# Optimization experiments

Hardware: AMD Instinct MI355X
Metric: run time of the kernel (lower is better)

The kernel has to match this reference:

```python
import jax, jax.numpy as jnp
import numpy as np

B = 1024          # number of graphs (subjects)
N1_PER = 116      # nodes per graph, branch 1 (AAL atlas)
N2_PER = 200      # nodes per graph, branch 2 (CC200 atlas)
DEG = 16          # sparsified adjacency degree
H = 32            # hidden_dim
NUM_CLASSES = 2


def _make_graph(key, b, n, deg):
    """Block-diagonal sparse adjacency in COO form, deg edges per node within its block."""
    N = b * n
    E = N * deg
    rows = jnp.repeat(jnp.arange(N, dtype=jnp.int32), deg)
    offs = jax.random.randint(jax.random.fold_in(key, 0), (E,), 0, n, dtype=jnp.int32)
    cols = (rows // n) * n + offs
    vals = jax.random.uniform(jax.random.fold_in(key, 1), (E,), dtype=jnp.float32)
    return rows, cols, vals


def setup_inputs() -> dict:
    key = jax.random.key(0)
    ks = jax.random.split(key, 20)
    rows1, cols1, vals1 = _make_graph(ks[0], B, N1_PER, DEG)
    rows2, cols2, vals2 = _make_graph(ks[1], B, N2_PER, DEG)
    x1 = jax.random.normal(ks[2], (B * N1_PER, N1_PER), dtype=jnp.float32)
    x2 = jax.random.normal(ks[3], (B * N2_PER, N2_PER), dtype=jnp.float32)
    s = 0.1
    inp = {
        "rows1": rows1, "cols1": cols1, "vals1": vals1, "x1": x1,
        "rows2": rows2, "cols2": cols2, "vals2": vals2, "x2": x2,
        # GCN branch 116
        "W1a": jax.random.normal(ks[4], (N1_PER, H), dtype=jnp.float32) * s,
        "b1a": jnp.zeros((H,), jnp.float32),
        "W1b": jax.random.normal(ks[5], (H, H), dtype=jnp.float32) * s,
        "b1b": jnp.zeros((H,), jnp.float32),
        # GCN branch 200
        "W2a": jax.random.normal(ks[6], (N2_PER, H), dtype=jnp.float32) * s,
        "b2a": jnp.zeros((H,), jnp.float32),
        "W2b": jax.random.normal(ks[7], (H, H), dtype=jnp.float32) * s,
        "b2b": jnp.zeros((H,), jnp.float32),
        # MLP head (stored as (in, out))
        "fc1_W": jax.random.normal(ks[8], (4 * H, H), dtype=jnp.float32) * s,
        "fc1_b": jnp.zeros((H,), jnp.float32),
        "fc2_W": jax.random.normal(ks[9], (H, H // 2), dtype=jnp.float32) * s,
        "fc2_b": jnp.zeros((H // 2,), jnp.float32),
        "fc3_W": jax.random.normal(ks[10], (H // 2, NUM_CLASSES), dtype=jnp.float32) * s,
        "fc3_b": jnp.zeros((NUM_CLASSES,), jnp.float32),
    }
    return inp


def _gcn(rows, cols, vals, x, W, b):
    # support = X @ W  (dense GEMM), then sparse aggregation A @ support, then bias
    support = x @ W                              # [N, H]
    msg = vals[:, None] * support[cols]          # gather + scale, [E, H]
    agg = jax.ops.segment_sum(msg, rows, num_segments=x.shape[0])  # scatter-add
    return agg + b


def _branch(rows, cols, vals, x, Wa, ba, Wb, bb, n_per):
    h = jax.nn.relu(_gcn(rows, cols, vals, x, Wa, ba))
    h = jax.nn.relu(_gcn(rows, cols, vals, h, Wb, bb))
    h = h.reshape(-1, n_per, h.shape[-1])        # [B, n, H]
    return jnp.concatenate([h.mean(axis=1), h.max(axis=1)], axis=1)  # [B, 2H]


def reference(rows1, cols1, vals1, x1, rows2, cols2, vals2, x2,
              W1a, b1a, W1b, b1b, W2a, b2a, W2b, b2b,
              fc1_W, fc1_b, fc2_W, fc2_b, fc3_W, fc3_b):
    f116 = _branch(rows1, cols1, vals1, x1, W1a, b1a, W1b, b1b, N1_PER)
    f200 = _branch(rows2, cols2, vals2, x2, W2a, b2a, W2b, b2b, N2_PER)
    x = jnp.concatenate([f116, f200], axis=1)    # [B, 4H]
    h = jax.nn.relu(x @ fc1_W + fc1_b)           # dropout is identity at inference
    h = jax.nn.relu(h @ fc2_W + fc2_b)
    logits = h @ fc3_W + fc3_b                   # [B, 2]
    return logits
```

## Files before the change

### kernel.cpp

```cpp
#include <hip/hip_runtime.h>

#define NB 1024
#define N1P 116
#define N2P 200
#define HD 32
#define T1 464
#define T2 800


template <int ST>
__device__ __forceinline__ void agg_phase(int base, int NPv,
                                          const int* __restrict__ cols,
                                          const float* __restrict__ vals,
                                          const float* __restrict__ sup,
                                          float bias, float* __restrict__ outh,
                                          int tid) {
    const int h = tid & 31;
    for (int n = tid >> 5; n < NPv; n += 8) {
        const int4* c4 = (const int4*)(cols + ((size_t)base + n) * 16);
        const float4* v4 = (const float4*)(vals + ((size_t)base + n) * 16);
        float a = bias;
#pragma unroll
        for (int q = 0; q < 4; ++q) {
            const int4 c = c4[q];
            const float4 v = v4[q];
            a += v.x * sup[(c.x - base) * ST + h];
            a += v.y * sup[(c.y - base) * ST + h];
            a += v.z * sup[(c.z - base) * ST + h];
            a += v.w * sup[(c.w - base) * ST + h];
        }
        outh[n * ST + h] = fmaxf(a, 0.f);
    }
}

template <int K>
__device__ void gemm1_tile(const float* __restrict__ xg,
                           const float* __restrict__ W,
                           float* __restrict__ Sout, float* sX) {
    constexpr int KC = 16;
    constexpr int SXS = 20;
    constexpr int NC = (K + KC - 1) / KC;
    const int tid = threadIdx.x;

    float acc[32];
#pragma unroll
    for (int c = 0; c < 32; ++c) acc[c] = 0.f;

    float4 cur[4];
    auto load_chunk = [&](int kc) {
        const int k0 = kc * KC;
        const int kw = (K - k0) < KC ? (K - k0) : KC;
        const int pieces = kw >> 2;
#pragma unroll
        for (int q = 0; q < 4; ++q) {
            const int i = tid + q * 256;
            const int row = i >> 2, p = i & 3;
            float4 v = make_float4(0.f, 0.f, 0.f, 0.f);
            if (p < pieces)
                v = *(const float4*)(xg + (size_t)row * K + k0 + p * 4);
            cur[q] = v;
        }
    };

    load_chunk(0);
#pragma unroll 1
    for (int kc = 0; kc < NC; ++kc) {
        float* sb = sX + (kc & 1) * (256 * SXS);
#pragma unroll
        for (int q = 0; q < 4; ++q) {
            const int i = tid + q * 256;
            *(float4*)&sb[(i >> 2) * SXS + (i & 3) * 4] = cur[q];
        }
        __syncthreads();
        if (kc + 1 < NC) load_chunk(kc + 1);
        const int k0 = kc * KC;
        const int kw = (K - k0) < KC ? (K - k0) : KC;
        const float* xrow = &sb[tid * SXS];
        const float* wb0 = W + (size_t)k0 * 32;
#pragma unroll 1
        for (int k4 = 0; k4 < kw; k4 += 4) {
            const float4 x4 = *(const float4*)&xrow[k4];
#pragma unroll
            for (int kk = 0; kk < 4; ++kk) {
                const float xs = (&x4.x)[kk];
                const float* w = wb0 + (k4 + kk) * 32;
#pragma unroll
                for (int c4 = 0; c4 < 8; ++c4) {
                    const float4 wv = *(const float4*)&w[c4 * 4];
                    acc[c4 * 4 + 0] += xs * wv.x;
                    acc[c4 * 4 + 1] += xs * wv.y;
                    acc[c4 * 4 + 2] += xs * wv.z;
                    acc[c4 * 4 + 3] += xs * wv.w;
                }
            }
        }
    }

    float* srow = Sout + (size_t)tid * 32;
#pragma unroll
    for (int c4 = 0; c4 < 8; ++c4) {
        float4 o;
        o.x = acc[c4 * 4 + 0]; o.y = acc[c4 * 4 + 1];
        o.z = acc[c4 * 4 + 2]; o.w = acc[c4 * 4 + 3];
        *(float4*)&srow[c4 * 4] = o;
    }
}

__global__ __launch_bounds__(256, 4) void gemm1_kernel(
        const float* __restrict__ x1, const float* __restrict__ W1a,
        float* __restrict__ S1,
        const float* __restrict__ x2, const float* __restrict__ W2a,
        float* __restrict__ S2) {
    __shared__ float sX[2 * 256 * 20];
    const int bid = blockIdx.x;
    if (bid < T1) {
        gemm1_tile<N1P>(x1 + (size_t)bid * 256 * N1P, W1a,
                        S1 + (size_t)bid * 256 * 32, sX);
    } else {
        const int t = bid - T1;
        gemm1_tile<N2P>(x2 + (size_t)t * 256 * N2P, W2a,
                        S2 + (size_t)t * 256 * 32, sX);
    }
}

template <int NP>
__device__ void graph_phase(int g, const float* __restrict__ S,
                            const int* __restrict__ cols,
                            const float* __restrict__ vals,
                            const float* __restrict__ ba,
                            const float* __restrict__ Wb,
                            const float* __restrict__ bb,
                            float* __restrict__ feats, int foff,
                            float* sSup, float* sH) {
    constexpr int ST = 33;
    const int tid = threadIdx.x;
    const int base = g * NP;
    const float bA = ba[tid & 31];
    const float bB = bb[tid & 31];

    const float* Sg = S + (size_t)base * 32;
    constexpr int PIECES = NP * 8;
    constexpr int PSL = (PIECES + 255) / 256;
#pragma unroll
    for (int q = 0; q < PSL; ++q) {
        const int i = tid + q * 256;
        if (i < PIECES) {
            const float4 v = *(const float4*)(Sg + (size_t)i * 4);
            *(float4*)&sSup[(i >> 3) * ST + (i & 7) * 4] = v;
        }
    }
    __syncthreads();

    agg_phase<ST>(base, NP, cols, vals, sSup, bA, sH, tid);
    __syncthreads();

    if (tid < NP) {
        float acc2[32];
#pragma unroll
        for (int c = 0; c < 32; ++c) acc2[c] = 0.f;
        const float* xrow = &sH[tid * ST];
#pragma unroll 1
        for (int k4 = 0; k4 < 32; k4 += 4) {
            const float4 x4 = *(const float4*)&xrow[k4];
#pragma unroll
            for (int kk = 0; kk < 4; ++kk) {
                const float xs = (&x4.x)[kk];
                const float* w = Wb + (k4 + kk) * 32;
#pragma unroll
                for (int c4 = 0; c4 < 8; ++c4) {
                    const float4 wv = *(const float4*)&w[c4 * 4];
                    acc2[c4 * 4 + 0] += xs * wv.x;
                    acc2[c4 * 4 + 1] += xs * wv.y;
                    acc2[c4 * 4 + 2] += xs * wv.z;
                    acc2[c4 * 4 + 3] += xs * wv.w;
                }
            }
        }
#pragma unroll
        for (int c4 = 0; c4 < 8; ++c4) {
            float4 o;
            o.x = acc2[c4 * 4 + 0]; o.y = acc2[c4 * 4 + 1];
            o.z = acc2[c4 * 4 + 2]; o.w = acc2[c4 * 4 + 3];
            *(float4*)&sSup[tid * ST + c4 * 4] = o;
        }
    }
    __syncthreads();

    agg_phase<ST>(base, NP, cols, vals, sSup, bB, sH, tid);
    __syncthreads();

    const int h = tid & 31, sl = tid >> 5;
    float sum = 0.f, mx = -1e30f;
    for (int n = sl; n < NP; n += 8) {
        const float v = sH[n * ST + h];
        sum += v;
        mx = fmaxf(mx, v);
    }
    float* sS = sSup;
    float* sM = sSup + 256;
    sS[tid] = sum;
    sM[tid] = mx;
    __syncthreads();
    if (tid < 32) {
#pragma unroll
        for (int q = 1; q < 8; ++q) {
            sum += sS[tid + 32 * q];
            mx = fmaxf(mx, sM[tid + 32 * q]);
        }
        feats[(size_t)g * 128 + foff + tid] = sum * (1.0f / NP);
        feats[(size_t)g * 128 + foff + 32 + tid] = mx;
    }
}

__global__ __launch_bounds__(256, 3) void graph_fused(
        const float* __restrict__ S1, const int* __restrict__ cols1,
        const float* __restrict__ vals1, const float* __restrict__ b1a,
        const float* __restrict__ W1b, const float* __restrict__ b1b,
        const float* __restrict__ S2, const int* __restrict__ cols2,
        const float* __restrict__ vals2, const float* __restrict__ b2a,
        const float* __restrict__ W2b, const float* __restrict__ b2b,
        float* __restrict__ feats) {
    __shared__ float sSup[N2P * 33];
    __shared__ float sH[N2P * 33];
    const int bid = blockIdx.x;
    const int g = bid >> 1;
    if ((bid & 1) == 0)
        graph_phase<N1P>(g, S1, cols1, vals1, b1a, W1b, b1b, feats, 0, sSup, sH);
    else
        graph_phase<N2P>(g, S2, cols2, vals2, b2a, W2b, b2b, feats, 64, sSup, sH);
}

template <int NP>
__device__ void branch_graph(int g,
                             const float* __restrict__ X,
                             const int* __restrict__ cols,
                             const float* __restrict__ vals,
                             const float* __restrict__ Wa,
                             const float* __restrict__ ba,
                             const float* __restrict__ Wb,
                             const float* __restrict__ bb,
                             float* __restrict__ feats, int foff,
                             float* sSup, float* sH) {
    constexpr int ST = 33;
    constexpr int KC = 16;
    constexpr int SXS = 20;
    constexpr int NSLOT = NP * 4;
    constexpr int PSL = (NSLOT + 255) / 256;

    const int tid = threadIdx.x;
    const int base = g * NP;
    const float* xg = X + (size_t)base * NP;
    const float bA = ba[tid & 31];
    const float bB = bb[tid & 31];

    float* sX = sSup;

    float acc[32];
#pragma unroll
    for (int c = 0; c < 32; ++c) acc[c] = 0.f;

    const int NC = (NP + KC - 1) / KC;

    float4 cur[PSL], nxt[PSL];

    auto load_chunk = [&](int kc, float4* buf) {
        const int k0 = kc * KC;
        const int kw = (NP - k0) < KC ? (NP - k0) : KC;
        const int pieces = kw >> 2;
#pragma unroll
        for (int q = 0; q < PSL; ++q) {
            const int i = tid + q * 256;
            float4 v = make_float4(0.f, 0.f, 0.f, 0.f);
            if (i < NSLOT) {
                const int row = i >> 2, p = i & 3;
                if (p < pieces)
                    v = *(const float4*)(xg + (size_t)row * NP + k0 + p * 4);
            }
            buf[q] = v;
        }
    };
    auto store_chunk = [&](const float4* buf) {
#pragma unroll
        for (int q = 0; q < PSL; ++q) {
            const int i = tid + q * 256;
            if (i < NSLOT) {
                const int row = i >> 2, p = i & 3;
                *(float4*)&sX[row * SXS + p * 4] = buf[q];
            }
        }
    };

    load_chunk(0, cur);
#pragma unroll 1
    for (int kc = 0; kc < NC; ++kc) {
        __syncthreads();
        store_chunk(cur);
        __syncthreads();
        if (kc + 1 < NC) load_chunk(kc + 1, nxt);
        const int k0 = kc * KC;
        const int kw = (NP - k0) < KC ? (NP - k0) : KC;
        if (tid < NP) {
            const float* xrow = &sX[tid * SXS];
            const float* wb0 = Wa + (size_t)k0 * 32;
#pragma unroll 1
            for (int k4 = 0; k4 < kw; k4 += 4) {
                const float4 x4 = *(const float4*)&xrow[k4];
#pragma unroll
                for (int kk = 0; kk < 4; ++kk) {
                    const float xs = (&x4.x)[kk];
                    const float* w = wb0 + (k4 + kk) * 32;
#pragma unroll
                    for (int c4 = 0; c4 < 8; ++c4) {
                        const float4 wv = *(const float4*)&w[c4 * 4];
                        acc[c4 * 4 + 0] += xs * wv.x;
                        acc[c4 * 4 + 1] += xs * wv.y;
                        acc[c4 * 4 + 2] += xs * wv.z;
                        acc[c4 * 4 + 3] += xs * wv.w;
                    }
                }
            }
        }
#pragma unroll
        for (int q = 0; q < PSL; ++q) cur[q] = nxt[q];
    }
    __syncthreads();

    if (tid < NP) {
#pragma unroll
        for (int c4 = 0; c4 < 8; ++c4) {
            float4 o;
            o.x = acc[c4 * 4 + 0]; o.y = acc[c4 * 4 + 1];
            o.z = acc[c4 * 4 + 2]; o.w = acc[c4 * 4 + 3];
            *(float4*)&sSup[tid * ST + c4 * 4] = o;
        }
    }
    __syncthreads();

    agg_phase<ST>(base, NP, cols, vals, sSup, bA, sH, tid);
    __syncthreads();

    if (tid < NP) {
        float acc2[32];
#pragma unroll
        for (int c = 0; c < 32; ++c) acc2[c] = 0.f;
        const float* xrow = &sH[tid * ST];
#pragma unroll 1
        for (int k4 = 0; k4 < 32; k4 += 4) {
            const float4 x4 = *(const float4*)&xrow[k4];
#pragma unroll
            for (int kk = 0; kk < 4; ++kk) {
                const float xs = (&x4.x)[kk];
                const float* w = Wb + (k4 + kk) * 32;
#pragma unroll
                for (int c4 = 0; c4 < 8; ++c4) {
                    const float4 wv = *(const float4*)&w[c4 * 4];
                    acc2[c4 * 4 + 0] += xs * wv.x;
                    acc2[c4 * 4 + 1] += xs * wv.y;
                    acc2[c4 * 4 + 2] += xs * wv.z;
                    acc2[c4 * 4 + 3] += xs * wv.w;
                }
            }
        }
#pragma unroll
        for (int c4 = 0; c4 < 8; ++c4) {
            float4 o;
            o.x = acc2[c4 * 4 + 0]; o.y = acc2[c4 * 4 + 1];
            o.z = acc2[c4 * 4 + 2]; o.w = acc2[c4 * 4 + 3];
            *(float4*)&sSup[tid * ST + c4 * 4] = o;
        }
    }
    __syncthreads();

    agg_phase<ST>(base, NP, cols, vals, sSup, bB, sH, tid);
    __syncthreads();

    const int h = tid & 31, sl = tid >> 5;
    float sum = 0.f, mx = -1e30f;
    for (int n = sl; n < NP; n += 8) {
        const float v = sH[n * ST + h];
        sum += v;
        mx = fmaxf(mx, v);
    }
    float* sS = sSup;
    float* sM = sSup + 256;
    sS[tid] = sum;
    sM[tid] = mx;
    __syncthreads();
    if (tid < 32) {
#pragma unroll
        for (int q = 1; q < 8; ++q) {
            sum += sS[tid + 32 * q];
            mx = fmaxf(mx, sM[tid + 32 * q]);
        }
        feats[(size_t)g * 128 + foff + tid] = sum * (1.0f / NP);
        feats[(size_t)g * 128 + foff + 32 + tid] = mx;
    }
}

__global__ __launch_bounds__(256, 3) void fused_branches(
        const float* __restrict__ x1, const int* __restrict__ cols1,
        const float* __restrict__ vals1,
        const float* __restrict__ W1a, const float* __restrict__ b1a,
        const float* __restrict__ W1b, const float* __restrict__ b1b,
        const float* __restrict__ x2, const int* __restrict__ cols2,
        const float* __restrict__ vals2,
        const float* __restrict__ W2a, const float* __restrict__ b2a,
        const float* __restrict__ W2b, const float* __restrict__ b2b,
        float* __restrict__ feats) {
    __shared__ float sSup[N2P * 33];
    __shared__ float sH[N2P * 33];
    const int bid = blockIdx.x;
    if (bid < NB) {
        branch_graph<N1P>(bid, x1, cols1, vals1, W1a, b1a, W1b, b1b, feats, 0,
                          sSup, sH);
    } else {
        branch_graph<N2P>(bid - NB, x2, cols2, vals2, W2a, b2a, W2b, b2b, feats,
                          64, sSup, sH);
    }
}

__global__ __launch_bounds__(256) void mlp_head(const float* __restrict__ feats,
                                                const float* __restrict__ W1,
                                                const float* __restrict__ b1,
                                                const float* __restrict__ W2,
                                                const float* __restrict__ b2,
                                                const float* __restrict__ W3,
                                                const float* __restrict__ b3,
                                                float* __restrict__ out) {
    __shared__ float sW1[128 * 32];
    __shared__ float sW2[32 * 16];
    __shared__ float sW3[16 * 2];
    __shared__ float sB1[32], sB2[16], sB3[2];
    __shared__ float sF[8 * 128];
    __shared__ float sH1[8 * 32];
    __shared__ float sH2[8 * 16];

    const int tid = threadIdx.x;
    for (int idx = tid; idx < 128 * 32; idx += 256) sW1[idx] = W1[idx];
    for (int idx = tid; idx < 32 * 16; idx += 256) sW2[idx] = W2[idx];
    if (tid < 32) { sW3[tid] = W3[tid]; sB1[tid] = b1[tid]; }
    if (tid < 16) sB2[tid] = b2[tid];
    if (tid < 2) sB3[tid] = b3[tid];
    const long g0 = (long)blockIdx.x * 8;
    for (int idx = tid; idx < 1024; idx += 256) sF[idx] = feats[g0 * 128 + idx];
    __syncthreads();

    const int g = tid >> 5, h = tid & 31;
    float a1 = sB1[h];
#pragma unroll 4
    for (int k = 0; k < 128; ++k) a1 += sF[g * 128 + k] * sW1[k * 32 + h];
    sH1[g * 32 + h] = fmaxf(a1, 0.f);
    __syncthreads();

    if (h < 16) {
        float a2 = sB2[h];
#pragma unroll
        for (int k = 0; k < 32; ++k) a2 += sH1[g * 32 + k] * sW2[k * 16 + h];
        sH2[g * 16 + h] = fmaxf(a2, 0.f);
    }
    __syncthreads();

    if (h < 2) {
        float a3 = sB3[h];
#pragma unroll
        for (int k = 0; k < 16; ++k) a3 += sH2[g * 16 + k] * sW3[k * 2 + h];
        out[(g0 + g) * 2 + h] = a3;
    }
}

extern "C" void kernel_launch(void* const* d_in, const int* in_sizes, int n_in,
                              void* d_out, int out_size, void* d_ws, size_t ws_size,
                              hipStream_t stream) {
    const int*   cols1 = (const int*)d_in[1];
    const float* vals1 = (const float*)d_in[2];
    const float* x1    = (const float*)d_in[3];
    const int*   cols2 = (const int*)d_in[5];
    const float* vals2 = (const float*)d_in[6];
    const float* x2    = (const float*)d_in[7];
    const float* W1a = (const float*)d_in[8];
    const float* b1a = (const float*)d_in[9];
    const float* W1b = (const float*)d_in[10];
    const float* b1b = (const float*)d_in[11];
    const float* W2a = (const float*)d_in[12];
    const float* b2a = (const float*)d_in[13];
    const float* W2b = (const float*)d_in[14];
    const float* b2b = (const float*)d_in[15];
    const float* fc1_W = (const float*)d_in[16];
    const float* fc1_b = (const float*)d_in[17];
    const float* fc2_W = (const float*)d_in[18];
    const float* fc2_b = (const float*)d_in[19];
    const float* fc3_W = (const float*)d_in[20];
    const float* fc3_b = (const float*)d_in[21];
    float* out = (float*)d_out;

    float* feats = (float*)d_ws;
    const size_t FEATS_N = (size_t)NB * 128;
    const size_t S1_N = (size_t)NB * N1P * 32;
    const size_t S2_N = (size_t)NB * N2P * 32;
    const size_t need = (FEATS_N + S1_N + S2_N) * sizeof(float);

    if (ws_size >= need) {
        float* S1 = feats + FEATS_N;
        float* S2 = S1 + S1_N;
        gemm1_kernel<<<T1 + T2, 256, 0, stream>>>(x1, W1a, S1, x2, W2a, S2);
        graph_fused<<<2 * NB, 256, 0, stream>>>(
            S1, cols1, vals1, b1a, W1b, b1b,
            S2, cols2, vals2, b2a, W2b, b2b, feats);
    } else {
        fused_branches<<<2 * NB, 256, 0, stream>>>(
            x1, cols1, vals1, W1a, b1a, W1b, b1b,
            x2, cols2, vals2, W2a, b2a, W2b, b2b, feats);
    }

    mlp_head<<<NB / 8, 256, 0, stream>>>(feats, fc1_W, fc1_b, fc2_W, fc2_b,
                                         fc3_W, fc3_b, out);
}
```

Before: 495.3 us.

## Use direct global-to-LDS loads in gemm1 and drop second LDS buffer in graph kernel

The first-layer GEMM now stages X tiles with global_load_lds (direct global-to-LDS DMA), using an XOR swizzle instead of padded rows and a register round-trip, and raises the occupancy hint. The graph kernel keeps first-layer aggregation results in registers, reuses one shared buffer instead of two, and fuses the second aggregation with the mean/max pooling. It also splits the sums into four independent accumulators. Halving shared memory lets more blocks fit per CU, at the cost of extra barriers and more register pressure.

Result: slower. 860.0 us (+73.6%).

```diff
diff --git a/kernel.cpp b/kernel.cpp
--- a/kernel.cpp
+++ b/kernel.cpp
@@ -1,4 +1,5 @@
 #include <hip/hip_runtime.h>
+#include <stdint.h>
 
 #define NB 1024
 #define N1P 116
@@ -8,29 +9,10 @@
 #define T2 800
 
 
-template <int ST>
-__device__ __forceinline__ void agg_phase(int base, int NPv,
-                                          const int* __restrict__ cols,
-                                          const float* __restrict__ vals,
-                                          const float* __restrict__ sup,
-                                          float bias, float* __restrict__ outh,
-                                          int tid) {
-    const int h = tid & 31;
-    for (int n = tid >> 5; n < NPv; n += 8) {
-        const int4* c4 = (const int4*)(cols + ((size_t)base + n) * 16);
-        const float4* v4 = (const float4*)(vals + ((size_t)base + n) * 16);
-        float a = bias;
-#pragma unroll
-        for (int q = 0; q < 4; ++q) {
-            const int4 c = c4[q];
-            const float4 v = v4[q];
-            a += v.x * sup[(c.x - base) * ST + h];
-            a += v.y * sup[(c.y - base) * ST + h];
-            a += v.z * sup[(c.z - base) * ST + h];
-            a += v.w * sup[(c.w - base) * ST + h];
-        }
-        outh[n * ST + h] = fmaxf(a, 0.f);
-    }
+__device__ __forceinline__ void gll16(const void* g, void* l) {
+    __builtin_amdgcn_global_load_lds(
+        (const __attribute__((address_space(1))) void*)g,
+        (__attribute__((address_space(3))) void*)l, 16, 0, 0);
 }
 
 template <int K>
@@ -38,62 +20,64 @@
                            const float* __restrict__ W,
                            float* __restrict__ Sout, float* sX) {
     constexpr int KC = 16;
-    constexpr int SXS = 20;
     constexpr int NC = (K + KC - 1) / KC;
     const int tid = threadIdx.x;
+    const int lane = tid & 63;
+    const int wave = tid >> 6;
+    const int ris = lane >> 2;
+    const int pq = lane & 3;
 
     float acc[32];
 #pragma unroll
     for (int c = 0; c < 32; ++c) acc[c] = 0.f;
 
-    float4 cur[4];
-    auto load_chunk = [&](int kc) {
+    auto issue = [&](int kc, int buf) {
+        const int k0 = kc * KC;
+        const int pieces = ((K - k0) < KC ? (K - k0) : KC) >> 2;
+#pragma unroll
+        for (int i = 0; i < 4; ++i) {
+            const int s = wave * 4 + i;
+            const int row = s * 16 + ris;
+            const int g = pq ^ ((row >> 1) & 3);
+            if (g < pieces)
+                gll16(xg + (size_t)row * K + k0 + g * 4,
+                      sX + buf * 4096 + s * 256);
+        }
+    };
+
+    issue(0, 0);
+    __syncthreads();
+
+    const int sw = (tid >> 1) & 3;
+    int buf = 0;
+#pragma unroll 1
+    for (int kc = 0; kc < NC; ++kc) {
+        if (kc + 1 < NC) issue(kc + 1, buf ^ 1);
         const int k0 = kc * KC;
         const int kw = (K - k0) < KC ? (K - k0) : KC;
-        const int pieces = kw >> 2;
-#pragma unroll
-        for (int q = 0; q < 4; ++q) {
-            const int i = tid + q * 256;
-            const int row = i >> 2, p = i & 3;
-            float4 v = make_float4(0.f, 0.f, 0.f, 0.f);
-            if (p < pieces)
-                v = *(const float4*)(xg + (size_t)row * K + k0 + p * 4);
-            cur[q] = v;
-        }
-    };
-
-    load_chunk(0);
-#pragma unroll 1
-    for (int kc = 0; kc < NC; ++kc) {
-        float* sb = sX + (kc & 1) * (256 * SXS);
-#pragma unroll
-        for (int q = 0; q < 4; ++q) {
-            const int i = tid + q * 256;
-            *(float4*)&sb[(i >> 2) * SXS + (i & 3) * 4] = cur[q];
+        const float* xrow = sX + buf * 4096 + tid * 16;
+#pragma unroll
+        for (int G = 0; G < 4; ++G) {
+            if (G * 4 < kw) {
+                const float4 x4 = *(const float4*)&xrow[(G ^ sw) * 4];
+                const float* wb = W + (size_t)(k0 + G * 4) * 32;
+#pragma unroll
+                for (int kk = 0; kk < 4; ++kk) {
+                    const float xs = (&x4.x)[kk];
+                    const float* w = wb + kk * 32;
+#pragma unroll
+                    for (int c4 = 0; c4 < 8; ++c4) {
+                        const float4 wv = *(const float4*)&w[c4 * 4];
+                        acc[c4 * 4 + 0] += xs * wv.x;
+                        acc[c4 * 4 + 1] += xs * wv.y;
+                        acc[c4 * 4 + 2] += xs * wv.z;
+                        acc[c4 * 4 + 3] += xs * wv.w;
+                    }
+                }
+            }
         }
         __syncthreads();
-        if (kc + 1 < NC) load_chunk(kc + 1);
-        const int k0 = kc * KC;
-        const int kw = (K - k0) < KC ? (K - k0) : KC;
-        const float* xrow = &sb[tid * SXS];
-        const float* wb0 = W + (size_t)k0 * 32;
-#pragma unroll 1
-        for (int k4 = 0; k4 < kw; k4 += 4) {
-            const float4 x4 = *(const float4*)&xrow[k4];
-#pragma unroll
-            for (int kk = 0; kk < 4; ++kk) {
-                const float xs = (&x4.x)[kk];
-                const float* w = wb0 + (k4 + kk) * 32;
-#pragma unroll
-                for (int c4 = 0; c4 < 8; ++c4) {
-                    const float4 wv = *(const float4*)&w[c4 * 4];
-                    acc[c4 * 4 + 0] += xs * wv.x;
-                    acc[c4 * 4 + 1] += xs * wv.y;
-                    acc[c4 * 4 + 2] += xs * wv.z;
-                    acc[c4 * 4 + 3] += xs * wv.w;
-                }
-            }
-        }
+        buf ^= 1;
     }
 
     float* srow = Sout + (size_t)tid * 32;
@@ -106,12 +90,12 @@
     }
 }
 
-__global__ __launch_bounds__(256, 4) void gemm1_kernel(
+__global__ __launch_bounds__(256, 5) void gemm1_kernel(
         const float* __restrict__ x1, const float* __restrict__ W1a,
         float* __restrict__ S1,
         const float* __restrict__ x2, const float* __restrict__ W2a,
         float* __restrict__ S2) {
-    __shared__ float sX[2 * 256 * 20];
+    __shared__ float sX[2 * 4096];
     const int bid = blockIdx.x;
     if (bid < T1) {
         gemm1_tile<N1P>(x1 + (size_t)bid * 256 * N1P, W1a,
@@ -131,12 +115,14 @@
                             const float* __restrict__ Wb,
                             const float* __restrict__ bb,
                             float* __restrict__ feats, int foff,
-                            float* sSup, float* sH) {
+                            float* sSup) {
     constexpr int ST = 33;
+    constexpr int NI = (NP + 7) / 8;
     const int tid = threadIdx.x;
+    const int h = tid & 31, sl = tid >> 5;
     const int base = g * NP;
-    const float bA = ba[tid & 31];
-    const float bB = bb[tid & 31];
+    const float bA = ba[h];
+    const float bB = bb[h];
 
     const float* Sg = S + (size_t)base * 32;
     constexpr int PIECES = NP * 8;
@@ -151,15 +137,41 @@
     }
     __syncthreads();
 
-    agg_phase<ST>(base, NP, cols, vals, sSup, bA, sH, tid);
-    __syncthreads();
-
+    float hr[NI];
+#pragma unroll
+    for (int i = 0; i < NI; ++i) {
+        const int n = sl + i * 8;
+        if (NP % 8 == 0 || n < NP) {
+            const int4* c4 = (const int4*)(cols + ((size_t)(base + n)) * 16);
+            const float4* v4 = (const float4*)(vals + ((size_t)(base + n)) * 16);
+            float a0 = 0.f, a1 = 0.f, a2 = 0.f, a3 = 0.f;
+#pragma unroll
+            for (int q = 0; q < 4; ++q) {
+                const int4 c = c4[q];
+                const float4 v = v4[q];
+                a0 += v.x * sSup[(c.x - base) * ST + h];
+                a1 += v.y * sSup[(c.y - base) * ST + h];
+                a2 += v.z * sSup[(c.z - base) * ST + h];
+                a3 += v.w * sSup[(c.w - base) * ST + h];
+            }
+            hr[i] = fmaxf(bA + ((a0 + a1) + (a2 + a3)), 0.f);
+        }
+    }
+    __syncthreads();
+
+#pragma unroll
+    for (int i = 0; i < NI; ++i) {
+        const int n = sl + i * 8;
+        if (NP % 8 == 0 || n < NP) sSup[n * ST + h] = hr[i];
+    }
+    __syncthreads();
+
+    float acc2[32];
     if (tid < NP) {
-        float acc2[32];
 #pragma unroll
         for (int c = 0; c < 32; ++c) acc2[c] = 0.f;
-        const float* xrow = &sH[tid * ST];
-#pragma unroll 1
+        const float* xrow = &sSup[tid * ST];
+#pragma unroll
         for (int k4 = 0; k4 < 32; k4 += 4) {
             const float4 x4 = *(const float4*)&xrow[k4];
 #pragma unroll
@@ -176,6 +188,10 @@
                 }
             }
         }
+    }
+    __syncthreads();
+
+    if (tid < NP) {
 #pragma unroll
         for (int c4 = 0; c4 < 8; ++c4) {
             float4 o;
@@ -186,33 +202,45 @@
     }
     __syncthreads();
 
-    agg_phase<ST>(base, NP, cols, vals, sSup, bB, sH, tid);
-    __syncthreads();
-
-    const int h = tid & 31, sl = tid >> 5;
     float sum = 0.f, mx = -1e30f;
-    for (int n = sl; n < NP; n += 8) {
-        const float v = sH[n * ST + h];
-        sum += v;
-        mx = fmaxf(mx, v);
-    }
-    float* sS = sSup;
-    float* sM = sSup + 256;
-    sS[tid] = sum;
-    sM[tid] = mx;
+#pragma unroll
+    for (int i = 0; i < NI; ++i) {
+        const int n = sl + i * 8;
+        if (NP % 8 == 0 || n < NP) {
+            const int4* c4 = (const int4*)(cols + ((size_t)(base + n)) * 16);
+            const float4* v4 = (const float4*)(vals + ((size_t)(base + n)) * 16);
+            float a0 = 0.f, a1 = 0.f, a2 = 0.f, a3 = 0.f;
+#pragma unroll
+            for (int q = 0; q < 4; ++q) {
+                const int4 c = c4[q];
+                const float4 v = v4[q];
+                a0 += v.x * sSup[(c.x - base) * ST + h];
+                a1 += v.y * sSup[(c.y - base) * ST + h];
+                a2 += v.z * sSup[(c.z - base) * ST + h];
+                a3 += v.w * sSup[(c.w - base) * ST + h];
+            }
+            const float v2 = fmaxf(bB + ((a0 + a1) + (a2 + a3)), 0.f);
+            sum += v2;
+            mx = fmaxf(mx, v2);
+        }
+    }
+    __syncthreads();
+
+    sSup[tid] = sum;
+    sSup[256 + tid] = mx;
     __syncthreads();
     if (tid < 32) {
 #pragma unroll
         for (int q = 1; q < 8; ++q) {
-            sum += sS[tid + 32 * q];
-            mx = fmaxf(mx, sM[tid + 32 * q]);
+            sum += sSup[tid + 32 * q];
+            mx = fmaxf(mx, sSup[256 + tid + 32 * q]);
         }
         feats[(size_t)g * 128 + foff + tid] = sum * (1.0f / NP);
         feats[(size_t)g * 128 + foff + 32 + tid] = mx;
     }
 }
 
-__global__ __launch_bounds__(256, 3) void graph_fused(
+__global__ __launch_bounds__(256, 6) void graph_fused(
         const float* __restrict__ S1, const int* __restrict__ cols1,
         const float* __restrict__ vals1, const float* __restrict__ b1a,
         const float* __restrict__ W1b, const float* __restrict__ b1b,
@@ -221,13 +249,37 @@
         const float* __restrict__ W2b, const float* __restrict__ b2b,
         float* __restrict__ feats) {
     __shared__ float sSup[N2P * 33];
-    __shared__ float sH[N2P * 33];
     const int bid = blockIdx.x;
     const int g = bid >> 1;
     if ((bid & 1) == 0)
-        graph_phase<N1P>(g, S1, cols1, vals1, b1a, W1b, b1b, feats, 0, sSup, sH);
+        graph_phase<N1P>(g, S1, cols1, vals1, b1a, W1b, b1b, feats, 0, sSup);
     else
-        graph_phase<N2P>(g, S2, cols2, vals2, b2a, W2b, b2b, feats, 64, sSup, sH);
+        graph_phase<N2P>(g, S2, cols2, vals2, b2a, W2b, b2b, feats, 64, sSup);
+}
+
+template <int ST>
+__device__ __forceinline__ void agg_phase_fb(int base, int NPv,
+                                             const int* __restrict__ cols,
+                                             const float* __restrict__ vals,
+                                             const float* __restrict__ sup,
+                                             float bias, float* __restrict__ outh,
+                                             int tid) {
+    const int h = tid & 31;
+    for (int n = tid >> 5; n < NPv; n += 8) {
+        const int4* c4 = (const int4*)(cols + ((size_t)base + n) * 16);
+        const float4* v4 = (const float4*)(vals + ((size_t)base + n) * 16);
+        float a = bias;
+#pragma unroll
+        for (int q = 0; q < 4; ++q) {
+            const int4 c = c4[q];
+            const float4 v = v4[q];
+            a += v.x * sup[(c.x - base) * ST + h];
+            a += v.y * sup[(c.y - base) * ST + h];
+            a += v.z * sup[(c.z - base) * ST + h];
+            a += v.w * sup[(c.w - base) * ST + h];
+        }
+        outh[n * ST + h] = fmaxf(a, 0.f);
+    }
 }
 
 template <int NP>
@@ -336,7 +388,7 @@
     }
     __syncthreads();
 
-    agg_phase<ST>(base, NP, cols, vals, sSup, bA, sH, tid);
+    agg_phase_fb<ST>(base, NP, cols, vals, sSup, bA, sH, tid);
     __syncthreads();
 
     if (tid < NP) {
@@ -371,7 +423,7 @@
     }
     __syncthreads();
 
-    agg_phase<ST>(base, NP, cols, vals, sSup, bB, sH, tid);
+    agg_phase_fb<ST>(base, NP, cols, vals, sSup, bB, sH, tid);
     __syncthreads();
 
     const int h = tid & 31, sl = tid >> 5;
```
